# Kernel optimization log

Hardware: AMD Instinct MI355X
Metric: run time of the kernel (lower is better)

Reference implementation:

```python
import jax, jax.numpy as jnp
import numpy as np

B, T, I = 8, 128, 196
TEXT_DIM, IMAGE_DIM, HIDDEN = 768, 1024, 512


def setup_inputs() -> dict:
    key = jax.random.key(0)
    ks = jax.random.split(key, 7)
    s = lambda d: 1.0 / np.sqrt(d)
    return {
        "text_features": jax.random.normal(ks[0], (B, T, TEXT_DIM), jnp.float32),
        "image_features": jax.random.normal(ks[1], (B, I, IMAGE_DIM), jnp.float32),
        "Wt": jax.random.normal(ks[2], (TEXT_DIM, HIDDEN), jnp.float32) * s(TEXT_DIM),
        "bt": jax.random.normal(ks[3], (HIDDEN,), jnp.float32) * s(TEXT_DIM),
        "Wi": jax.random.normal(ks[4], (IMAGE_DIM, HIDDEN), jnp.float32) * s(IMAGE_DIM),
        "bi": jax.random.normal(ks[5], (HIDDEN,), jnp.float32) * s(IMAGE_DIM),
        "wa": jax.random.normal(ks[6], (HIDDEN,), jnp.float32) * s(HIDDEN),
        "ba": jnp.zeros((1,), jnp.float32),
    }


def reference(text_features, image_features, Wt, bt, Wi, bi, wa, ba):
    # projections: [B,T,H] and [B,I,H]
    pt = jnp.einsum("btd,dh->bth", text_features, Wt) + bt
    pi = jnp.einsum("bid,dh->bih", image_features, Wi) + bi
    # additive Bahdanau scores: tanh of broadcast sum [B,T,I,H], reduced by wa
    h = jnp.tanh(pt[:, :, None, :] + pi[:, None, :, :])
    scores = jnp.einsum("btih,h->bti", h, wa) + ba[0]  # [B,T,I]
    text_attended = jnp.einsum("bti,bid->btd", jax.nn.softmax(scores, axis=-1), image_features)
    image_attended = jnp.einsum("bti,btd->bid", jax.nn.softmax(scores, axis=1), text_features)
    return text_attended, image_attended
```

## Files before the change

### kernel.cpp

```cpp
#include <hip/hip_runtime.h>
#include <math.h>

#define B 8
#define T 128
#define I_TOK 196
#define TEXT_DIM 768
#define IMAGE_DIM 1024
#define HIDDEN 512
#define EXP_SCALE 2.88539008177792681f

#if __has_builtin(__builtin_amdgcn_exp2f)
#define FAST_EXP2(x) __builtin_amdgcn_exp2f(x)
#else
#define FAST_EXP2(x) exp2f(x)
#endif
#if __has_builtin(__builtin_amdgcn_rcpf)
#define FAST_RCP(x) __builtin_amdgcn_rcpf(x)
#else
#define FAST_RCP(x) __fdividef(1.f, (x))
#endif
#if __has_builtin(__builtin_amdgcn_sched_barrier)
#define SCHED_FENCE() __builtin_amdgcn_sched_barrier(0)
#else
#define SCHED_FENCE()
#endif

typedef short bf16x8 __attribute__((ext_vector_type(8)));
typedef float f32x4 __attribute__((ext_vector_type(4)));

#define KT_T (TEXT_DIM / 32)
#define KT_I (IMAGE_DIM / 32)
#define MT_T (B * T / 16)
#define MT_I (B * I_TOK / 16)
#define NT   (HIDDEN / 16)

#define XT_ELEMS (MT_T * KT_T * 512)
#define XI_ELEMS (MT_I * KT_I * 512)
#define X_ELEMS  (XT_ELEMS + XI_ELEMS)
#define WT_T_ELEMS (NT * KT_T * 512)
#define W_ELEMS (WT_T_ELEMS + NT * KT_I * 512)

#define XTILES_T (MT_T * KT_T)
#define XTILES   (XTILES_T + MT_I * KT_I)
#define WTILES_T (NT * KT_T)
#define WTILES   (WTILES_T + NT * KT_I)
#define PREP_GRID ((XTILES + WTILES) / 4)

__device__ __forceinline__ unsigned short f2bf(float x) {
    unsigned int u = __float_as_uint(x);
    unsigned int r = u + 0x7FFFu + ((u >> 16) & 1u);
    return (unsigned short)(r >> 16);
}
__device__ __forceinline__ float bf2f(unsigned short h) {
    return __uint_as_float(((unsigned int)h) << 16);
}

__global__ __launch_bounds__(256) void prep_kernel(
        const float* __restrict__ text, const float* __restrict__ image,
        const float* __restrict__ Wt, const float* __restrict__ Wi,
        unsigned short* __restrict__ Xh, unsigned short* __restrict__ Xl,
        unsigned short* __restrict__ WTh, unsigned short* __restrict__ WTl)
{
    const int tid = threadIdx.x;
    const int lane = tid & 63, wv = tid >> 6;
    const int r16 = lane & 15, quad = lane >> 4;
    const int id = blockIdx.x * 4 + wv;

    float v[8];
    unsigned short* oh;
    unsigned short* ol;
    long dst;

    if (id < XTILES) {
        const float* X; int K, mt, kt;
        if (id < XTILES_T) { X = text; K = TEXT_DIM; mt = id / KT_T; kt = id % KT_T; }
        else { const int i2 = id - XTILES_T; X = image; K = IMAGE_DIM; mt = i2 / KT_I; kt = i2 % KT_I; }
        const float* src = X + (long)(mt * 16 + r16) * K + kt * 32 + quad * 8;
        const float4 a = *(const float4*)src;
        const float4 b = *(const float4*)(src + 4);
        v[0]=a.x; v[1]=a.y; v[2]=a.z; v[3]=a.w; v[4]=b.x; v[5]=b.y; v[6]=b.z; v[7]=b.w;
        oh = (id < XTILES_T) ? Xh : Xh + XT_ELEMS;
        ol = (id < XTILES_T) ? Xl : Xl + XT_ELEMS;
        const long tile = (id < XTILES_T) ? id : (long)(id - XTILES_T);
        dst = tile * 512 + lane * 8;
    } else {
        const int idw = id - XTILES;
        const float* W; int K, nt, kt;
        if (idw < WTILES_T) { W = Wt; K = TEXT_DIM; nt = idw / KT_T; kt = idw % KT_T; }
        else { const int i2 = idw - WTILES_T; W = Wi; K = IMAGE_DIM; nt = i2 / KT_I; kt = i2 % KT_I; }
        const float* src = W + (long)(kt * 32 + quad * 8) * HIDDEN + nt * 16 + r16;
        #pragma unroll
        for (int j = 0; j < 8; ++j) v[j] = src[(long)j * HIDDEN];
        oh = (idw < WTILES_T) ? WTh : WTh + WT_T_ELEMS;
        ol = (idw < WTILES_T) ? WTl : WTl + WT_T_ELEMS;
        const long tile = (idw < WTILES_T) ? idw : (long)(idw - WTILES_T);
        dst = tile * 512 + lane * 8;
    }

    uint4 hv, lv;
    unsigned int hh[8], ll[8];
    #pragma unroll
    for (int j = 0; j < 8; ++j) {
        hh[j] = f2bf(v[j]);
        ll[j] = f2bf(v[j] - bf2f((unsigned short)hh[j]));
    }
    hv.x = hh[0] | (hh[1] << 16); hv.y = hh[2] | (hh[3] << 16);
    hv.z = hh[4] | (hh[5] << 16); hv.w = hh[6] | (hh[7] << 16);
    lv.x = ll[0] | (ll[1] << 16); lv.y = ll[2] | (ll[3] << 16);
    lv.z = ll[4] | (ll[5] << 16); lv.w = ll[6] | (ll[7] << 16);
    *(uint4*)(oh + dst) = hv;
    *(uint4*)(ol + dst) = lv;
}

#define GT_BLOCKS (32 * 8)
#define GI_BLOCKS (49 * 8)
#define GEMM_GRID (GT_BLOCKS + GI_BLOCKS)
#define PSTRIDE 66

__global__ __launch_bounds__(256, 2) void mfma_proj_kernel(
        const unsigned short* __restrict__ Xh, const unsigned short* __restrict__ Xl,
        const unsigned short* __restrict__ WTh, const unsigned short* __restrict__ WTl,
        const float* __restrict__ bt, const float* __restrict__ bi,
        float* __restrict__ pt, float* __restrict__ pi)
{
    __shared__ float part[32 * PSTRIDE];

    const int tid = threadIdx.x;
    const int lane = tid & 63, wv = tid >> 6;
    const int r16 = lane & 15, quad = lane >> 4;
    const int nh = wv & 1;
    const int kh = wv >> 1;

    int bid = blockIdx.x;
    const unsigned short *xh, *xl, *wh, *wl; const float* bias; float* Y;
    int ktiles;
    if (bid < GT_BLOCKS) {
        xh = Xh; xl = Xl; wh = WTh; wl = WTl; bias = bt; Y = pt; ktiles = KT_T;
    } else {
        bid -= GT_BLOCKS;
        xh = Xh + XT_ELEMS; xl = Xl + XT_ELEMS;
        wh = WTh + WT_T_ELEMS; wl = WTl + WT_T_ELEMS;
        bias = bi; Y = pi; ktiles = KT_I;
    }
    const int m0 = (bid >> 3) * 32;
    const int n0 = (bid & 7) * 64 + nh * 32;
    const int nstep = ktiles >> 1;
    const int kt0 = kh * nstep;
    const int mt0 = (bid >> 3) * 2;
    const int nt0 = (bid & 7) * 4 + nh * 2;

    const unsigned short* pa0 = xh + ((long)mt0 * ktiles + kt0) * 512 + lane * 8;
    const unsigned short* pa1 = pa0 + (long)ktiles * 512;
    const unsigned short* qa0 = xl + ((long)mt0 * ktiles + kt0) * 512 + lane * 8;
    const unsigned short* qa1 = qa0 + (long)ktiles * 512;
    const unsigned short* pb0 = wh + ((long)nt0 * ktiles + kt0) * 512 + lane * 8;
    const unsigned short* pb1 = pb0 + (long)ktiles * 512;
    const unsigned short* qb0 = wl + ((long)nt0 * ktiles + kt0) * 512 + lane * 8;
    const unsigned short* qb1 = qb0 + (long)ktiles * 512;

    f32x4 a00 = {0,0,0,0}, a01 = {0,0,0,0}, a10 = {0,0,0,0}, a11 = {0,0,0,0};

    bf16x8 Ah0 = *(const bf16x8*)(pa0);
    bf16x8 Ah1 = *(const bf16x8*)(pa1);
    bf16x8 Al0 = *(const bf16x8*)(qa0);
    bf16x8 Al1 = *(const bf16x8*)(qa1);
    bf16x8 Bh0 = *(const bf16x8*)(pb0);
    bf16x8 Bh1 = *(const bf16x8*)(pb1);
    bf16x8 Bl0 = *(const bf16x8*)(qb0);
    bf16x8 Bl1 = *(const bf16x8*)(qb1);

    for (int s = 0; s < nstep; ++s) {
        const long kn = (s + 1 < nstep) ? (long)(s + 1) * 512 : 0;
        const bf16x8 nAh0 = *(const bf16x8*)(pa0 + kn);
        const bf16x8 nAh1 = *(const bf16x8*)(pa1 + kn);
        const bf16x8 nAl0 = *(const bf16x8*)(qa0 + kn);
        const bf16x8 nAl1 = *(const bf16x8*)(qa1 + kn);
        const bf16x8 nBh0 = *(const bf16x8*)(pb0 + kn);
        const bf16x8 nBh1 = *(const bf16x8*)(pb1 + kn);
        const bf16x8 nBl0 = *(const bf16x8*)(qb0 + kn);
        const bf16x8 nBl1 = *(const bf16x8*)(qb1 + kn);
        SCHED_FENCE();

        a00 = __builtin_amdgcn_mfma_f32_16x16x32_bf16(Ah0, Bh0, a00, 0, 0, 0);
        a01 = __builtin_amdgcn_mfma_f32_16x16x32_bf16(Ah0, Bh1, a01, 0, 0, 0);
        a10 = __builtin_amdgcn_mfma_f32_16x16x32_bf16(Ah1, Bh0, a10, 0, 0, 0);
        a11 = __builtin_amdgcn_mfma_f32_16x16x32_bf16(Ah1, Bh1, a11, 0, 0, 0);
        a00 = __builtin_amdgcn_mfma_f32_16x16x32_bf16(Ah0, Bl0, a00, 0, 0, 0);
        a01 = __builtin_amdgcn_mfma_f32_16x16x32_bf16(Ah0, Bl1, a01, 0, 0, 0);
        a10 = __builtin_amdgcn_mfma_f32_16x16x32_bf16(Ah1, Bl0, a10, 0, 0, 0);
        a11 = __builtin_amdgcn_mfma_f32_16x16x32_bf16(Ah1, Bl1, a11, 0, 0, 0);
        a00 = __builtin_amdgcn_mfma_f32_16x16x32_bf16(Al0, Bh0, a00, 0, 0, 0);
        a01 = __builtin_amdgcn_mfma_f32_16x16x32_bf16(Al0, Bh1, a01, 0, 0, 0);
        a10 = __builtin_amdgcn_mfma_f32_16x16x32_bf16(Al1, Bh0, a10, 0, 0, 0);
        a11 = __builtin_amdgcn_mfma_f32_16x16x32_bf16(Al1, Bh1, a11, 0, 0, 0);
        SCHED_FENCE();

        Ah0 = nAh0; Ah1 = nAh1; Al0 = nAl0; Al1 = nAl1;
        Bh0 = nBh0; Bh1 = nBh1; Bl0 = nBl0; Bl1 = nBl1;
    }

    const int lc = nh * 32 + r16;
    if (kh == 1) {
        #pragma unroll
        for (int r = 0; r < 4; ++r) {
            part[(quad * 4 + r) * PSTRIDE + lc]           = a00[r];
            part[(quad * 4 + r) * PSTRIDE + lc + 16]      = a01[r];
            part[(quad * 4 + 16 + r) * PSTRIDE + lc]      = a10[r];
            part[(quad * 4 + 16 + r) * PSTRIDE + lc + 16] = a11[r];
        }
    }
    __syncthreads();
    if (kh == 0) {
        const int row0 = m0 + quad * 4;
        const float bv0 = bias[n0 + r16];
        const float bv1 = bias[n0 + 16 + r16];
        #pragma unroll
        for (int r = 0; r < 4; ++r) {
            const float v00 = (a00[r] + part[(quad * 4 + r) * PSTRIDE + lc]           + bv0) * EXP_SCALE;
            const float v01 = (a01[r] + part[(quad * 4 + r) * PSTRIDE + lc + 16]      + bv1) * EXP_SCALE;
            const float v10 = (a10[r] + part[(quad * 4 + 16 + r) * PSTRIDE + lc]      + bv0) * EXP_SCALE;
            const float v11 = (a11[r] + part[(quad * 4 + 16 + r) * PSTRIDE + lc + 16] + bv1) * EXP_SCALE;
            Y[(long)(row0 + r)      * HIDDEN + n0 + r16]      = FAST_EXP2(v00);
            Y[(long)(row0 + r)      * HIDDEN + n0 + 16 + r16] = FAST_EXP2(v01);
            Y[(long)(row0 + 16 + r) * HIDDEN + n0 + r16]      = FAST_EXP2(v10);
            Y[(long)(row0 + 16 + r) * HIDDEN + n0 + 16 + r16] = FAST_EXP2(v11);
        }
    }
}

__global__ __launch_bounds__(256, 4) void scores_kernel(const float* __restrict__ pt,
        const float* __restrict__ pi, const float* __restrict__ wa,
        const float* __restrict__ ba, float* __restrict__ scores)
{
    const int blk = blockIdx.x;
    const int half = blk & 1;
    const int bt0 = (blk >> 1) * 2;
    const int b = bt0 >> 7;
    const int tid = threadIdx.x;
    const int lane = tid & 63, wave = tid >> 6;

    const float* ptrow = pt + (long)bt0 * HIDDEN + lane * 8;
    const float4 pA0 = *(const float4*)ptrow;
    const float4 pB0 = *(const float4*)(ptrow + 4);
    const float4 pA1 = *(const float4*)(ptrow + HIDDEN);
    const float4 pB1 = *(const float4*)(ptrow + HIDDEN + 4);
    float4 wA = *(const float4*)(wa + lane * 8);
    float4 wB = *(const float4*)(wa + lane * 8 + 4);

    float S = wA.x + wA.y + wA.z + wA.w + wB.x + wB.y + wB.z + wB.w;
    #pragma unroll
    for (int off = 32; off; off >>= 1) S += __shfl_down(S, off);
    const float base = S + ba[0];

    wA.x *= -2.f; wA.y *= -2.f; wA.z *= -2.f; wA.w *= -2.f;
    wB.x *= -2.f; wB.y *= -2.f; wB.z *= -2.f; wB.w *= -2.f;

    const float* pib = pi + (long)b * I_TOK * HIDDEN + lane * 8;
    const int i0 = half * 98 + wave;
    const int iend = half * 98 + 98;

    float4 ca = *(const float4*)(pib + (long)i0 * HIDDEN);
    float4 cb = *(const float4*)(pib + (long)i0 * HIDDEN + 4);

    for (int i = i0; i < iend; i += 4) {
        const int inx = (i + 4 < iend) ? (i + 4) : i;
        const float4 na = *(const float4*)(pib + (long)inx * HIDDEN);
        const float4 nb = *(const float4*)(pib + (long)inx * HIDDEN + 4);

        float acc0 = 0.f;
        acc0 = fmaf(wA.x, FAST_RCP(fmaf(pA0.x, ca.x, 1.f)), acc0);
        acc0 = fmaf(wA.y, FAST_RCP(fmaf(pA0.y, ca.y, 1.f)), acc0);
        acc0 = fmaf(wA.z, FAST_RCP(fmaf(pA0.z, ca.z, 1.f)), acc0);
        acc0 = fmaf(wA.w, FAST_RCP(fmaf(pA0.w, ca.w, 1.f)), acc0);
        acc0 = fmaf(wB.x, FAST_RCP(fmaf(pB0.x, cb.x, 1.f)), acc0);
        acc0 = fmaf(wB.y, FAST_RCP(fmaf(pB0.y, cb.y, 1.f)), acc0);
        acc0 = fmaf(wB.z, FAST_RCP(fmaf(pB0.z, cb.z, 1.f)), acc0);
        acc0 = fmaf(wB.w, FAST_RCP(fmaf(pB0.w, cb.w, 1.f)), acc0);

        float acc1 = 0.f;
        acc1 = fmaf(wA.x, FAST_RCP(fmaf(pA1.x, ca.x, 1.f)), acc1);
        acc1 = fmaf(wA.y, FAST_RCP(fmaf(pA1.y, ca.y, 1.f)), acc1);
        acc1 = fmaf(wA.z, FAST_RCP(fmaf(pA1.z, ca.z, 1.f)), acc1);
        acc1 = fmaf(wA.w, FAST_RCP(fmaf(pA1.w, ca.w, 1.f)), acc1);
        acc1 = fmaf(wB.x, FAST_RCP(fmaf(pB1.x, cb.x, 1.f)), acc1);
        acc1 = fmaf(wB.y, FAST_RCP(fmaf(pB1.y, cb.y, 1.f)), acc1);
        acc1 = fmaf(wB.z, FAST_RCP(fmaf(pB1.z, cb.z, 1.f)), acc1);
        acc1 = fmaf(wB.w, FAST_RCP(fmaf(pB1.w, cb.w, 1.f)), acc1);

        #pragma unroll
        for (int off = 32; off; off >>= 1) {
            acc0 += __shfl_down(acc0, off);
            acc1 += __shfl_down(acc1, off);
        }
        if (lane == 0) {
            scores[(long)bt0 * I_TOK + i]       = base + acc0;
            scores[(long)(bt0 + 1) * I_TOK + i] = base + acc1;
        }
        ca = na; cb = nb;
    }
}

#define ATT_P1_BLOCKS 256
#define ATT_P2_BLOCKS (B * 28)
#define ATT_GRID (ATT_P1_BLOCKS + ATT_P2_BLOCKS)

__global__ __launch_bounds__(256) void att_kernel(const float* __restrict__ scores,
        const float* __restrict__ image, const float* __restrict__ text,
        float* __restrict__ out_text, float* __restrict__ out_img)
{
    const int tid = threadIdx.x, lane = tid & 63, wave = tid >> 6;

    if (blockIdx.x < ATT_P1_BLOCKS) {
        const int bid = blockIdx.x;
        const int csplit = bid & 1;
        const int grp = bid >> 1;
        const int b = grp >> 4;
        const int t0 = (grp & 15) * 8;

        __shared__ float ps[I_TOK][8];
        #pragma unroll
        for (int rr = 0; rr < 2; ++rr) {
            const int tsub = wave + rr * 4;
            const float* srow = scores + ((long)(b * T + t0 + tsub)) * I_TOK;
            const float s0 = srow[lane];
            const float s1 = srow[lane + 64];
            const float s2 = srow[lane + 128];
            const float s3 = (lane < 4) ? srow[lane + 192] : -INFINITY;
            float m = fmaxf(fmaxf(s0, s1), fmaxf(s2, s3));
            #pragma unroll
            for (int off = 32; off; off >>= 1) m = fmaxf(m, __shfl_xor(m, off));
            const float e0 = __expf(s0 - m);
            const float e1 = __expf(s1 - m);
            const float e2 = __expf(s2 - m);
            const float e3 = (lane < 4) ? __expf(s3 - m) : 0.f;
            float sum = e0 + e1 + e2 + e3;
            #pragma unroll
            for (int off = 32; off; off >>= 1) sum += __shfl_xor(sum, off);
            const float inv = __fdividef(1.0f, sum);
            ps[lane][tsub] = e0 * inv;
            ps[lane + 64][tsub] = e1 * inv;
            ps[lane + 128][tsub] = e2 * inv;
            if (lane < 4) ps[lane + 192][tsub] = e3 * inv;
        }
        __syncthreads();

        const float* img = image + (long)b * I_TOK * IMAGE_DIM + csplit * 512 + tid * 2;
        float2 a0 = {0,0}, a1 = {0,0}, a2 = {0,0}, a3 = {0,0};
        float2 a4 = {0,0}, a5 = {0,0}, a6 = {0,0}, a7 = {0,0};

        float2 v0 = *(const float2*)(img + 0 * IMAGE_DIM);
        float2 v1 = *(const float2*)(img + 1 * IMAGE_DIM);
        float2 v2 = *(const float2*)(img + 2 * IMAGE_DIM);
        float2 v3 = *(const float2*)(img + 3 * IMAGE_DIM);
        float4 pL0 = *(const float4*)&ps[0][0]; float4 pH0 = *(const float4*)&ps[0][4];
        float4 pL1 = *(const float4*)&ps[1][0]; float4 pH1 = *(const float4*)&ps[1][4];
        float4 pL2 = *(const float4*)&ps[2][0]; float4 pH2 = *(const float4*)&ps[2][4];
        float4 pL3 = *(const float4*)&ps[3][0]; float4 pH3 = *(const float4*)&ps[3][4];

        for (int g = 0; g < 49; ++g) {
            const int ib = (g + 1 < 49) ? (g + 1) * 4 : g * 4;
            const float2 w0 = *(const float2*)(img + (long)(ib + 0) * IMAGE_DIM);
            const float2 w1 = *(const float2*)(img + (long)(ib + 1) * IMAGE_DIM);
            const float2 w2 = *(const float2*)(img + (long)(ib + 2) * IMAGE_DIM);
            const float2 w3 = *(const float2*)(img + (long)(ib + 3) * IMAGE_DIM);
            const float4 nL0 = *(const float4*)&ps[ib + 0][0]; const float4 nH0 = *(const float4*)&ps[ib + 0][4];
            const float4 nL1 = *(const float4*)&ps[ib + 1][0]; const float4 nH1 = *(const float4*)&ps[ib + 1][4];
            const float4 nL2 = *(const float4*)&ps[ib + 2][0]; const float4 nH2 = *(const float4*)&ps[ib + 2][4];
            const float4 nL3 = *(const float4*)&ps[ib + 3][0]; const float4 nH3 = *(const float4*)&ps[ib + 3][4];

#define ATT_ROW(vr, pl, ph)                                                   \
            a0.x = fmaf(pl.x, vr.x, a0.x); a0.y = fmaf(pl.x, vr.y, a0.y);     \
            a1.x = fmaf(pl.y, vr.x, a1.x); a1.y = fmaf(pl.y, vr.y, a1.y);     \
            a2.x = fmaf(pl.z, vr.x, a2.x); a2.y = fmaf(pl.z, vr.y, a2.y);     \
            a3.x = fmaf(pl.w, vr.x, a3.x); a3.y = fmaf(pl.w, vr.y, a3.y);     \
            a4.x = fmaf(ph.x, vr.x, a4.x); a4.y = fmaf(ph.x, vr.y, a4.y);     \
            a5.x = fmaf(ph.y, vr.x, a5.x); a5.y = fmaf(ph.y, vr.y, a5.y);     \
            a6.x = fmaf(ph.z, vr.x, a6.x); a6.y = fmaf(ph.z, vr.y, a6.y);     \
            a7.x = fmaf(ph.w, vr.x, a7.x); a7.y = fmaf(ph.w, vr.y, a7.y);
            ATT_ROW(v0, pL0, pH0)
            ATT_ROW(v1, pL1, pH1)
            ATT_ROW(v2, pL2, pH2)
            ATT_ROW(v3, pL3, pH3)
#undef ATT_ROW
            v0 = w0; v1 = w1; v2 = w2; v3 = w3;
            pL0 = nL0; pH0 = nH0; pL1 = nL1; pH1 = nH1;
            pL2 = nL2; pH2 = nH2; pL3 = nL3; pH3 = nH3;
        }
        float* o = out_text + ((long)(b * T + t0)) * IMAGE_DIM + csplit * 512 + tid * 2;
        *(float2*)(o + 0 * IMAGE_DIM) = a0;
        *(float2*)(o + 1 * IMAGE_DIM) = a1;
        *(float2*)(o + 2 * IMAGE_DIM) = a2;
        *(float2*)(o + 3 * IMAGE_DIM) = a3;
        *(float2*)(o + 4 * IMAGE_DIM) = a4;
        *(float2*)(o + 5 * IMAGE_DIM) = a5;
        *(float2*)(o + 6 * IMAGE_DIM) = a6;
        *(float2*)(o + 7 * IMAGE_DIM) = a7;
    } else {
        const int bid = blockIdx.x - ATT_P1_BLOCKS;
        const int b = bid / 28;
        const int i0 = (bid % 28) * 7;

        __shared__ float qs[T][8];
        for (int cc = wave; cc < 7; cc += 4) {
            const float* sc = scores + (long)b * T * I_TOK + (i0 + cc);
            const float s0 = sc[(long)lane * I_TOK];
            const float s1 = sc[(long)(lane + 64) * I_TOK];
            float m = fmaxf(s0, s1);
            #pragma unroll
            for (int off = 32; off; off >>= 1) m = fmaxf(m, __shfl_xor(m, off));
            const float e0 = __expf(s0 - m);
            const float e1 = __expf(s1 - m);
            float sum = e0 + e1;
            #pragma unroll
            for (int off = 32; off; off >>= 1) sum += __shfl_xor(sum, off);
            const float inv = __fdividef(1.0f, sum);
            qs[lane][cc] = e0 * inv;
            qs[lane + 64][cc] = e1 * inv;
        }
        __syncthreads();

        const float* txt2 = text + (long)b * T * TEXT_DIM + tid * 2;
        const float* txt1 = text + (long)b * T * TEXT_DIM + 512 + tid;
        float ax[7], ay[7], az[7];
        #pragma unroll
        for (int r = 0; r < 7; ++r) { ax[r] = 0.f; ay[r] = 0.f; az[r] = 0.f; }

        float2 u0 = *(const float2*)(txt2 + 0 * TEXT_DIM);
        float2 u1 = *(const float2*)(txt2 + 1 * TEXT_DIM);
        float  z0 = txt1[0 * TEXT_DIM];
        float  z1 = txt1[1 * TEXT_DIM];
        float4 qa0 = *(const float4*)&qs[0][0]; float4 qb0 = *(const float4*)&qs[0][4];
        float4 qa1 = *(const float4*)&qs[1][0]; float4 qb1 = *(const float4*)&qs[1][4];

        for (int g = 0; g < 64; ++g) {
            const int tb = (g + 1 < 64) ? (g + 1) * 2 : g * 2;
            const float2 nu0 = *(const float2*)(txt2 + (long)(tb + 0) * TEXT_DIM);
            const float2 nu1 = *(const float2*)(txt2 + (long)(tb + 1) * TEXT_DIM);
            const float  nz0 = txt1[(long)(tb + 0) * TEXT_DIM];
            const float  nz1 = txt1[(long)(tb + 1) * TEXT_DIM];
            const float4 na0 = *(const float4*)&qs[tb + 0][0];
            const float4 nb0 = *(const float4*)&qs[tb + 0][4];
            const float4 na1 = *(const float4*)&qs[tb + 1][0];
            const float4 nb1 = *(const float4*)&qs[tb + 1][4];

            ax[0] = fmaf(qa0.x, u0.x, ax[0]); ay[0] = fmaf(qa0.x, u0.y, ay[0]); az[0] = fmaf(qa0.x, z0, az[0]);
            ax[1] = fmaf(qa0.y, u0.x, ax[1]); ay[1] = fmaf(qa0.y, u0.y, ay[1]); az[1] = fmaf(qa0.y, z0, az[1]);
            ax[2] = fmaf(qa0.z, u0.x, ax[2]); ay[2] = fmaf(qa0.z, u0.y, ay[2]); az[2] = fmaf(qa0.z, z0, az[2]);
            ax[3] = fmaf(qa0.w, u0.x, ax[3]); ay[3] = fmaf(qa0.w, u0.y, ay[3]); az[3] = fmaf(qa0.w, z0, az[3]);
            ax[4] = fmaf(qb0.x, u0.x, ax[4]); ay[4] = fmaf(qb0.x, u0.y, ay[4]); az[4] = fmaf(qb0.x, z0, az[4]);
            ax[5] = fmaf(qb0.y, u0.x, ax[5]); ay[5] = fmaf(qb0.y, u0.y, ay[5]); az[5] = fmaf(qb0.y, z0, az[5]);
            ax[6] = fmaf(qb0.z, u0.x, ax[6]); ay[6] = fmaf(qb0.z, u0.y, ay[6]); az[6] = fmaf(qb0.z, z0, az[6]);
            ax[0] = fmaf(qa1.x, u1.x, ax[0]); ay[0] = fmaf(qa1.x, u1.y, ay[0]); az[0] = fmaf(qa1.x, z1, az[0]);
            ax[1] = fmaf(qa1.y, u1.x, ax[1]); ay[1] = fmaf(qa1.y, u1.y, ay[1]); az[1] = fmaf(qa1.y, z1, az[1]);
            ax[2] = fmaf(qa1.z, u1.x, ax[2]); ay[2] = fmaf(qa1.z, u1.y, ay[2]); az[2] = fmaf(qa1.z, z1, az[2]);
            ax[3] = fmaf(qa1.w, u1.x, ax[3]); ay[3] = fmaf(qa1.w, u1.y, ay[3]); az[3] = fmaf(qa1.w, z1, az[3]);
            ax[4] = fmaf(qb1.x, u1.x, ax[4]); ay[4] = fmaf(qb1.x, u1.y, ay[4]); az[4] = fmaf(qb1.x, z1, az[4]);
            ax[5] = fmaf(qb1.y, u1.x, ax[5]); ay[5] = fmaf(qb1.y, u1.y, ay[5]); az[5] = fmaf(qb1.y, z1, az[5]);
            ax[6] = fmaf(qb1.z, u1.x, ax[6]); ay[6] = fmaf(qb1.z, u1.y, ay[6]); az[6] = fmaf(qb1.z, z1, az[6]);

            u0 = nu0; u1 = nu1; z0 = nz0; z1 = nz1;
            qa0 = na0; qb0 = nb0; qa1 = na1; qb1 = nb1;
        }
        float* o = out_img + ((long)b * I_TOK + i0) * TEXT_DIM;
        #pragma unroll
        for (int r = 0; r < 7; ++r) {
            float2 w;
            w.x = ax[r]; w.y = ay[r];
            *(float2*)(o + (long)r * TEXT_DIM + tid * 2) = w;
            o[(long)r * TEXT_DIM + 512 + tid] = az[r];
        }
    }
}

extern "C" void kernel_launch(void* const* d_in, const int* in_sizes, int n_in,
                              void* d_out, int out_size, void* d_ws, size_t ws_size,
                              hipStream_t stream) {
    const float* text  = (const float*)d_in[0];
    const float* image = (const float*)d_in[1];
    const float* Wt    = (const float*)d_in[2];
    const float* bt    = (const float*)d_in[3];
    const float* Wi    = (const float*)d_in[4];
    const float* bi    = (const float*)d_in[5];
    const float* wa    = (const float*)d_in[6];
    const float* ba    = (const float*)d_in[7];

    float* pt = (float*)d_ws;
    float* pi = pt + (long)B * T * HIDDEN;
    float* sc = pi + (long)B * I_TOK * HIDDEN;
    unsigned short* Xh  = (unsigned short*)(sc + (long)B * T * I_TOK);
    unsigned short* Xl  = Xh + X_ELEMS;
    unsigned short* WTh = Xl + X_ELEMS;
    unsigned short* WTl = WTh + W_ELEMS;

    float* out_text = (float*)d_out;
    float* out_img  = out_text + (long)B * T * IMAGE_DIM;

    prep_kernel<<<PREP_GRID, 256, 0, stream>>>(text, image, Wt, Wi, Xh, Xl, WTh, WTl);
    mfma_proj_kernel<<<GEMM_GRID, 256, 0, stream>>>(Xh, Xl, WTh, WTl, bt, bi, pt, pi);
    scores_kernel<<<B * T, 256, 0, stream>>>(pt, pi, wa, ba, sc);
    att_kernel<<<ATT_GRID, 256, 0, stream>>>(sc, image, text, out_text, out_img);
}
```

Measured before the change: 144.9 us.

## Stage projection GEMM tiles through LDS with async global-to-LDS loads

Measured after the change: 142.4 us. Within noise of the previous version (-1.7%).

```diff
diff --git a/kernel.cpp b/kernel.cpp
--- a/kernel.cpp
+++ b/kernel.cpp
@@ -19,14 +19,12 @@
 #else
 #define FAST_RCP(x) __fdividef(1.f, (x))
 #endif
-#if __has_builtin(__builtin_amdgcn_sched_barrier)
-#define SCHED_FENCE() __builtin_amdgcn_sched_barrier(0)
-#else
-#define SCHED_FENCE()
-#endif
 
 typedef short bf16x8 __attribute__((ext_vector_type(8)));
 typedef float f32x4 __attribute__((ext_vector_type(4)));
+
+typedef __attribute__((address_space(3))) void       as3_void;
+typedef __attribute__((address_space(1))) const void as1_cvoid;
 
 #define KT_T (TEXT_DIM / 32)
 #define KT_I (IMAGE_DIM / 32)
@@ -112,10 +110,9 @@
     *(uint4*)(ol + dst) = lv;
 }
 
-#define GT_BLOCKS (32 * 8)
-#define GI_BLOCKS (49 * 8)
-#define GEMM_GRID (GT_BLOCKS + GI_BLOCKS)
-#define PSTRIDE 66
+#define GT2_BLOCKS (16 * 8)
+#define GI2_BLOCKS (25 * 8)
+#define GEMM_GRID (GT2_BLOCKS + GI2_BLOCKS)
 
 __global__ __launch_bounds__(256, 2) void mfma_proj_kernel(
         const unsigned short* __restrict__ Xh, const unsigned short* __restrict__ Xl,
@@ -123,63 +120,72 @@
         const float* __restrict__ bt, const float* __restrict__ bi,
         float* __restrict__ pt, float* __restrict__ pi)
 {
-    __shared__ float part[32 * PSTRIDE];
+    __shared__ __align__(16) unsigned short lds[2][16][512];
 
     const int tid = threadIdx.x;
     const int lane = tid & 63, wv = tid >> 6;
     const int r16 = lane & 15, quad = lane >> 4;
-    const int nh = wv & 1;
-    const int kh = wv >> 1;
-
-    int bid = blockIdx.x;
+    const int wr = wv >> 1, wc = wv & 1;
+
+    const int bid0 = blockIdx.x;
+    int bid;
+    if (bid0 < GT2_BLOCKS) bid = (bid0 & 7) * 16 + (bid0 >> 3);
+    else { const int d = bid0 - GT2_BLOCKS; bid = GT2_BLOCKS + (d & 7) * 25 + (d >> 3); }
+
     const unsigned short *xh, *xl, *wh, *wl; const float* bias; float* Y;
-    int ktiles;
-    if (bid < GT_BLOCKS) {
+    int ktiles, mt0;
+    int n8;
+    if (bid < GT2_BLOCKS) {
         xh = Xh; xl = Xl; wh = WTh; wl = WTl; bias = bt; Y = pt; ktiles = KT_T;
+        mt0 = (bid >> 3) * 4; n8 = bid & 7;
     } else {
-        bid -= GT_BLOCKS;
+        const int ib = bid - GT2_BLOCKS;
         xh = Xh + XT_ELEMS; xl = Xl + XT_ELEMS;
         wh = WTh + WT_T_ELEMS; wl = WTl + WT_T_ELEMS;
         bias = bi; Y = pi; ktiles = KT_I;
-    }
-    const int m0 = (bid >> 3) * 32;
-    const int n0 = (bid & 7) * 64 + nh * 32;
-    const int nstep = ktiles >> 1;
-    const int kt0 = kh * nstep;
-    const int mt0 = (bid >> 3) * 2;
-    const int nt0 = (bid & 7) * 4 + nh * 2;
-
-    const unsigned short* pa0 = xh + ((long)mt0 * ktiles + kt0) * 512 + lane * 8;
-    const unsigned short* pa1 = pa0 + (long)ktiles * 512;
-    const unsigned short* qa0 = xl + ((long)mt0 * ktiles + kt0) * 512 + lane * 8;
-    const unsigned short* qa1 = qa0 + (long)ktiles * 512;
-    const unsigned short* pb0 = wh + ((long)nt0 * ktiles + kt0) * 512 + lane * 8;
-    const unsigned short* pb1 = pb0 + (long)ktiles * 512;
-    const unsigned short* qb0 = wl + ((long)nt0 * ktiles + kt0) * 512 + lane * 8;
-    const unsigned short* qb1 = qb0 + (long)ktiles * 512;
+        const int mg = ib >> 3;
+        mt0 = (mg == 24) ? (MT_I - 4) : mg * 4;
+        n8 = ib & 7;
+    }
+    const int nt0 = n8 * 4;
+
+    const unsigned short* ssrc[4];
+    #pragma unroll
+    for (int q = 0; q < 4; ++q) {
+        const int t = wv * 4 + q;
+        const int g = t >> 2;
+        const int i = t & 3;
+        const unsigned short* base = (g == 0) ? xh : (g == 1) ? xl : (g == 2) ? wh : wl;
+        const long row = (g < 2) ? (long)(mt0 + i) : (long)(nt0 + i);
+        ssrc[q] = base + row * ktiles * 512 + lane * 8;
+    }
+
+#define STAGE(buf, kt) do {                                                    \
+        _Pragma("unroll")                                                      \
+        for (int q_ = 0; q_ < 4; ++q_) {                                       \
+            __builtin_amdgcn_global_load_lds(                                  \
+                (as1_cvoid*)(ssrc[q_] + (long)(kt) * 512),                     \
+                (as3_void*)&lds[buf][wv * 4 + q_][0], 16, 0, 0);               \
+        } } while (0)
 
     f32x4 a00 = {0,0,0,0}, a01 = {0,0,0,0}, a10 = {0,0,0,0}, a11 = {0,0,0,0};
 
-    bf16x8 Ah0 = *(const bf16x8*)(pa0);
-    bf16x8 Ah1 = *(const bf16x8*)(pa1);
-    bf16x8 Al0 = *(const bf16x8*)(qa0);
-    bf16x8 Al1 = *(const bf16x8*)(qa1);
-    bf16x8 Bh0 = *(const bf16x8*)(pb0);
-    bf16x8 Bh1 = *(const bf16x8*)(pb1);
-    bf16x8 Bl0 = *(const bf16x8*)(qb0);
-    bf16x8 Bl1 = *(const bf16x8*)(qb1);
-
-    for (int s = 0; s < nstep; ++s) {
-        const long kn = (s + 1 < nstep) ? (long)(s + 1) * 512 : 0;
-        const bf16x8 nAh0 = *(const bf16x8*)(pa0 + kn);
-        const bf16x8 nAh1 = *(const bf16x8*)(pa1 + kn);
-        const bf16x8 nAl0 = *(const bf16x8*)(qa0 + kn);
-        const bf16x8 nAl1 = *(const bf16x8*)(qa1 + kn);
-        const bf16x8 nBh0 = *(const bf16x8*)(pb0 + kn);
-        const bf16x8 nBh1 = *(const bf16x8*)(pb1 + kn);
-        const bf16x8 nBl0 = *(const bf16x8*)(qb0 + kn);
-        const bf16x8 nBl1 = *(const bf16x8*)(qb1 + kn);
-        SCHED_FENCE();
+    STAGE(0, 0);
+    __syncthreads();
+
+    int cur = 0;
+    for (int s = 0; s < ktiles; ++s) {
+        if (s + 1 < ktiles) STAGE(cur ^ 1, s + 1);
+
+        const int fo = lane * 8;
+        const bf16x8 Ah0 = *(const bf16x8*)&lds[cur][wr * 2 + 0][fo];
+        const bf16x8 Ah1 = *(const bf16x8*)&lds[cur][wr * 2 + 1][fo];
+        const bf16x8 Al0 = *(const bf16x8*)&lds[cur][4 + wr * 2 + 0][fo];
+        const bf16x8 Al1 = *(const bf16x8*)&lds[cur][4 + wr * 2 + 1][fo];
+        const bf16x8 Bh0 = *(const bf16x8*)&lds[cur][8 + wc * 2 + 0][fo];
+        const bf16x8 Bh1 = *(const bf16x8*)&lds[cur][8 + wc * 2 + 1][fo];
+        const bf16x8 Bl0 = *(const bf16x8*)&lds[cur][12 + wc * 2 + 0][fo];
+        const bf16x8 Bl1 = *(const bf16x8*)&lds[cur][12 + wc * 2 + 1][fo];
 
         a00 = __builtin_amdgcn_mfma_f32_16x16x32_bf16(Ah0, Bh0, a00, 0, 0, 0);
         a01 = __builtin_amdgcn_mfma_f32_16x16x32_bf16(Ah0, Bh1, a01, 0, 0, 0);
@@ -193,38 +199,22 @@
         a01 = __builtin_amdgcn_mfma_f32_16x16x32_bf16(Al0, Bh1, a01, 0, 0, 0);
         a10 = __builtin_amdgcn_mfma_f32_16x16x32_bf16(Al1, Bh0, a10, 0, 0, 0);
         a11 = __builtin_amdgcn_mfma_f32_16x16x32_bf16(Al1, Bh1, a11, 0, 0, 0);
-        SCHED_FENCE();
-
-        Ah0 = nAh0; Ah1 = nAh1; Al0 = nAl0; Al1 = nAl1;
-        Bh0 = nBh0; Bh1 = nBh1; Bl0 = nBl0; Bl1 = nBl1;
-    }
-
-    const int lc = nh * 32 + r16;
-    if (kh == 1) {
-        #pragma unroll
-        for (int r = 0; r < 4; ++r) {
-            part[(quad * 4 + r) * PSTRIDE + lc]           = a00[r];
-            part[(quad * 4 + r) * PSTRIDE + lc + 16]      = a01[r];
-            part[(quad * 4 + 16 + r) * PSTRIDE + lc]      = a10[r];
-            part[(quad * 4 + 16 + r) * PSTRIDE + lc + 16] = a11[r];
-        }
-    }
-    __syncthreads();
-    if (kh == 0) {
-        const int row0 = m0 + quad * 4;
-        const float bv0 = bias[n0 + r16];
-        const float bv1 = bias[n0 + 16 + r16];
-        #pragma unroll
-        for (int r = 0; r < 4; ++r) {
-            const float v00 = (a00[r] + part[(quad * 4 + r) * PSTRIDE + lc]           + bv0) * EXP_SCALE;
-            const float v01 = (a01[r] + part[(quad * 4 + r) * PSTRIDE + lc + 16]      + bv1) * EXP_SCALE;
-            const float v10 = (a10[r] + part[(quad * 4 + 16 + r) * PSTRIDE + lc]      + bv0) * EXP_SCALE;
-            const float v11 = (a11[r] + part[(quad * 4 + 16 + r) * PSTRIDE + lc + 16] + bv1) * EXP_SCALE;
-            Y[(long)(row0 + r)      * HIDDEN + n0 + r16]      = FAST_EXP2(v00);
-            Y[(long)(row0 + r)      * HIDDEN + n0 + 16 + r16] = FAST_EXP2(v01);
-            Y[(long)(row0 + 16 + r) * HIDDEN + n0 + r16]      = FAST_EXP2(v10);
-            Y[(long)(row0 + 16 + r) * HIDDEN + n0 + 16 + r16] = FAST_EXP2(v11);
-        }
+
+        __syncthreads();
+        cur ^= 1;
+    }
+#undef STAGE
+
+    const int row00 = (mt0 + wr * 2) * 16 + quad * 4;
+    const int col0  = (nt0 + wc * 2) * 16 + r16;
+    const float bv0 = bias[col0];
+    const float bv1 = bias[col0 + 16];
+    #pragma unroll
+    for (int r = 0; r < 4; ++r) {
+        Y[(long)(row00 + r)      * HIDDEN + col0]      = FAST_EXP2((a00[r] + bv0) * EXP_SCALE);
+        Y[(long)(row00 + r)      * HIDDEN + col0 + 16] = FAST_EXP2((a01[r] + bv1) * EXP_SCALE);
+        Y[(long)(row00 + 16 + r) * HIDDEN + col0]      = FAST_EXP2((a10[r] + bv0) * EXP_SCALE);
+        Y[(long)(row00 + 16 + r) * HIDDEN + col0 + 16] = FAST_EXP2((a11[r] + bv1) * EXP_SCALE);
     }
 }
 
```
